# Kernel optimization log

Hardware: AMD Instinct MI355X
Metric: run time of the kernel (lower is better)

Reference implementation:

```python
import jax, jax.numpy as jnp
import numpy as np

N = 20000      # nodes
E = 320000     # directed edges (avg degree 16)
H = 4          # GAT attention heads
IN, HID, OUT = 5, 64, 32
DIMS = [(HID, HID), (HID, HID), (HID, OUT)]  # per-layer (in, out_per_head)


def setup_inputs() -> dict:
    keys = iter(jax.random.split(jax.random.key(0), 64))

    def rn(shape, s=0.1):
        return jax.random.normal(next(keys), shape, jnp.float32) * s

    inp = {
        "x": jax.random.normal(next(keys), (N, IN), jnp.float32),
        "edge_index": jax.random.randint(next(keys), (2, E), 0, N, dtype=jnp.int32),
        "enc_W": rn((IN, HID)), "enc_b": rn((HID,)),
    }
    for l, (din, dout) in enumerate(DIMS):
        inp["W%d" % l] = rn((din, H * dout))
        inp["as%d" % l] = rn((H, dout))
        inp["ad%d" % l] = rn((H, dout))
        inp["b%d" % l] = rn((dout,))
        inp["g%d" % l] = 1.0 + rn((dout,))
        inp["be%d" % l] = rn((dout,))
        inp["m%d" % l] = rn((dout,))
        inp["v%d" % l] = 1.0 + 0.1 * jax.random.uniform(next(keys), (dout,), jnp.float32)
    for h in ("eth", "man"):
        inp[h + "_W1"] = rn((OUT, OUT // 2)); inp[h + "_b1"] = rn((OUT // 2,))
        inp[h + "_W2"] = rn((OUT // 2, 1)); inp[h + "_b2"] = rn((1,))
    return inp


def _gat(x, src, dst, W, a_s, a_d, bias, n):
    # PyG GATConv: heads=H, concat=False (head mean), leaky_relu slope 0.2
    xp = (x @ W).reshape(n, H, -1)                        # [N,H,C]
    al_s = (xp * a_s).sum(-1)                             # [N,H]
    al_d = (xp * a_d).sum(-1)                             # [N,H]
    e = jax.nn.leaky_relu(al_s[src] + al_d[dst], 0.2)     # [E',H]
    emax = jax.ops.segment_max(e, dst, num_segments=n)    # stable softmax over in-edges
    ee = jnp.exp(e - emax[dst])
    den = jax.ops.segment_sum(ee, dst, num_segments=n)
    alpha = ee / (den[dst] + 1e-16)                       # [E',H]
    out = jax.ops.segment_sum(alpha[:, :, None] * xp[src], dst, num_segments=n)
    return out.mean(axis=1) + bias                        # [N,C]


def _bn(x, g, b, m, v):
    # BatchNorm1d, eval mode with running stats
    return (x - m) / jnp.sqrt(v + 1e-5) * g + b


def _head(z, W1, b1, W2, b2):
    # Linear -> ReLU -> (dropout off) -> Linear -> Sigmoid
    return jax.nn.sigmoid(jax.nn.relu(z @ W1 + b1) @ W2 + b2)


def _forward(x, src, dst, enc_W, enc_b, Ws, ASs, ADs, Bs, Gs, BEs, Ms, Vs, eth, man):
    n = x.shape[0]
    h = x @ enc_W + enc_b
    for l in range(3):
        h = _gat(h, src, dst, Ws[l], ASs[l], ADs[l], Bs[l], n)
        h = _bn(h, Gs[l], BEs[l], Ms[l], Vs[l])
        if l < 2:
            h = jax.nn.relu(h)
    graph_emb = h.mean(axis=0, keepdims=True)             # no `batch` attr branch
    ethics = _head(graph_emb, *eth)
    manip = _head(graph_emb, *man)
    return h, graph_emb, ethics, manip


def reference(x, edge_index, enc_W, enc_b,
              W0, as0, ad0, b0, g0, be0, m0, v0,
              W1, as1, ad1, b1, g1, be1, m1, v1,
              W2, as2, ad2, b2, g2, be2, m2, v2,
              eth_W1, eth_b1, eth_W2, eth_b2,
              man_W1, man_b1, man_W2, man_b2):
    n = x.shape[0]
    loops = jnp.arange(n, dtype=edge_index.dtype)
    src = jnp.concatenate([edge_index[0], loops])         # GATConv adds self-loops
    dst = jnp.concatenate([edge_index[1], loops])
    return _forward(x, src, dst, enc_W, enc_b,
                    [W0, W1, W2], [as0, as1, as2], [ad0, ad1, ad2], [b0, b1, b2],
                    [g0, g1, g2], [be0, be1, be2], [m0, m1, m2], [v0, v1, v2],
                    (eth_W1, eth_b1, eth_W2, eth_b2),
                    (man_W1, man_b1, man_W2, man_b2))
```

## Files before the change

### kernel.cpp

```cpp
#include <hip/hip_runtime.h>
#include <math.h>


#define H4 4

static __device__ __forceinline__ unsigned short f2bf(float f) {
  unsigned u = __float_as_uint(f);
  u += 0x7fffu + ((u >> 16) & 1u);
  return (unsigned short)(u >> 16);
}

static __device__ __forceinline__ float bfh(unsigned u) {
  return __uint_as_float(u << 16);
}
static __device__ __forceinline__ float bfl(unsigned u) {
  return __uint_as_float(u & 0xffff0000u);
}

__global__ void k_count(const int* __restrict__ dst, int* __restrict__ deg, int E) {
  int gid = blockIdx.x * blockDim.x + threadIdx.x;
  if (gid < E) atomicAdd(&deg[dst[gid]], 1);
}

__global__ void k_alloc(int* __restrict__ cursor, int* __restrict__ rbeg,
                        int* __restrict__ rend, int* __restrict__ col,
                        int* __restrict__ counter, float* __restrict__ gacc, int N) {
  int gid = blockIdx.x * blockDim.x + threadIdx.x;
  int lane = threadIdx.x & 63;
  if (gid < 32) gacc[gid] = 0.f;
  int size = (gid < N) ? (cursor[gid] + 1) : 0;
  int v = size;
#pragma unroll
  for (int off = 1; off < 64; off <<= 1) {
    int t = __shfl_up(v, off, 64);
    if (lane >= off) v += t;
  }
  int tot = __shfl(v, 63, 64);
  int base = 0;
  if (lane == 63) base = atomicAdd(counter, tot);
  base = __shfl(base, 63, 64);
  if (gid < N) {
    int p = base + v - size;
    rbeg[gid] = p;
    rend[gid] = p + size;
    col[p] = gid;
    cursor[gid] = p + 1;
  }
}

__global__ void k_scatter(const int* __restrict__ src, const int* __restrict__ dst,
                          int* __restrict__ cursor, int* __restrict__ col, int E) {
  int gid = blockIdx.x * blockDim.x + threadIdx.x;
  if (gid < E) {
    int p = atomicAdd(&cursor[dst[gid]], 1);
    col[p] = src[gid];
  }
}

template <int HC, bool ENC>
__global__ void k_gemm_al(const float* __restrict__ hin,
                          const float* __restrict__ encW, const float* __restrict__ encb,
                          const float* __restrict__ W,
                          const float* __restrict__ a_s, const float* __restrict__ a_d,
                          unsigned short* __restrict__ xpb,
                          float* __restrict__ als, float* __restrict__ ald, int N) {
  constexpr int K = 64, NB = 16, C = HC / H4;
  __shared__ float hs[NB * K];
  int n0 = blockIdx.x * NB;
  int tid = threadIdx.x;
  if (ENC) {
    for (int idx = tid; idx < NB * K; idx += HC) {
      int i = idx >> 6, j = idx & 63;
      int n = n0 + i;
      float a = 0.f;
      if (n < N) {
        a = encb[j];
#pragma unroll
        for (int k = 0; k < 5; ++k) a += hin[n * 5 + k] * encW[k * 64 + j];
      }
      hs[idx] = a;
    }
  } else {
    for (int idx = tid; idx < NB * K; idx += HC) {
      int n = n0 + (idx >> 6);
      hs[idx] = (n < N) ? hin[(size_t)n0 * K + idx] : 0.f;
    }
  }
  __syncthreads();
  float acc[NB];
#pragma unroll
  for (int i = 0; i < NB; ++i) acc[i] = 0.f;
  for (int k = 0; k < K; k += 4) {
    float w0 = W[(k + 0) * HC + tid];
    float w1 = W[(k + 1) * HC + tid];
    float w2 = W[(k + 2) * HC + tid];
    float w3 = W[(k + 3) * HC + tid];
#pragma unroll
    for (int i = 0; i < NB; ++i) {
      float4 hv = *(const float4*)&hs[i * K + k];
      acc[i] += hv.x * w0 + hv.y * w1 + hv.z * w2 + hv.w * w3;
    }
  }
#pragma unroll
  for (int i = 0; i < NB; ++i) {
    int n = n0 + i;
    if (n < N) xpb[(size_t)n * HC + tid] = f2bf(acc[i]);
  }
  float as_w = a_s[tid], ad_w = a_d[tid];
  int c = tid & (C - 1);
  int h = tid / C;
#pragma unroll
  for (int i = 0; i < NB; ++i) {
    float vs = acc[i] * as_w, vd = acc[i] * ad_w;
#pragma unroll
    for (int off = C >> 1; off; off >>= 1) {
      vs += __shfl_xor(vs, off, 64);
      vd += __shfl_xor(vd, off, 64);
    }
    int n = n0 + i;
    if (c == 0 && n < N) {
      als[n * H4 + h] = vs;
      ald[n * H4 + h] = vd;
    }
  }
}

template <int C, bool RELU>
__global__ void k_gather(const unsigned short* __restrict__ xpb,
                         const float* __restrict__ als, const float* __restrict__ ald,
                         const int* __restrict__ rbeg, const int* __restrict__ rend,
                         const int* __restrict__ col,
                         const float* __restrict__ bias, const float* __restrict__ g,
                         const float* __restrict__ be, const float* __restrict__ m,
                         const float* __restrict__ v, float* __restrict__ hout, int N) {
  constexpr int HC = H4 * C;
  constexpr int VPL = HC / 64;
  int wave = threadIdx.x >> 6;
  int lane = threadIdx.x & 63;
  int n = blockIdx.x * 2 + wave;
  if (n >= N) return;
  int h = lane >> 4;
  float aldn = ald[n * H4 + h];
  int beg = rbeg[n], end = rend[n];

  float s = 0.f;
  float acc[VPL];
#pragma unroll
  for (int i = 0; i < VPL; ++i) acc[i] = 0.f;

  int j = beg;
  for (; j + 3 < end; j += 4) {
    int s0 = col[j], s1 = col[j + 1], s2 = col[j + 2], s3 = col[j + 3];
    float a0 = als[s0 * H4 + h], a1 = als[s1 * H4 + h];
    float a2 = als[s2 * H4 + h], a3 = als[s3 * H4 + h];
    float e0 = a0 + aldn; e0 = (e0 > 0.f) ? e0 : 0.2f * e0; e0 = __expf(e0);
    float e1 = a1 + aldn; e1 = (e1 > 0.f) ? e1 : 0.2f * e1; e1 = __expf(e1);
    float e2 = a2 + aldn; e2 = (e2 > 0.f) ? e2 : 0.2f * e2; e2 = __expf(e2);
    float e3 = a3 + aldn; e3 = (e3 > 0.f) ? e3 : 0.2f * e3; e3 = __expf(e3);
    s += (e0 + e1) + (e2 + e3);
    if constexpr (VPL == 4) {
      uint2 u0 = *(const uint2*)(xpb + (size_t)s0 * HC + lane * 4);
      uint2 u1 = *(const uint2*)(xpb + (size_t)s1 * HC + lane * 4);
      uint2 u2 = *(const uint2*)(xpb + (size_t)s2 * HC + lane * 4);
      uint2 u3 = *(const uint2*)(xpb + (size_t)s3 * HC + lane * 4);
      acc[0] += e0 * bfh(u0.x) + e1 * bfh(u1.x) + e2 * bfh(u2.x) + e3 * bfh(u3.x);
      acc[1] += e0 * bfl(u0.x) + e1 * bfl(u1.x) + e2 * bfl(u2.x) + e3 * bfl(u3.x);
      acc[2] += e0 * bfh(u0.y) + e1 * bfh(u1.y) + e2 * bfh(u2.y) + e3 * bfh(u3.y);
      acc[3] += e0 * bfl(u0.y) + e1 * bfl(u1.y) + e2 * bfl(u2.y) + e3 * bfl(u3.y);
    } else {
      unsigned u0 = *(const unsigned*)(xpb + (size_t)s0 * HC + lane * 2);
      unsigned u1 = *(const unsigned*)(xpb + (size_t)s1 * HC + lane * 2);
      unsigned u2 = *(const unsigned*)(xpb + (size_t)s2 * HC + lane * 2);
      unsigned u3 = *(const unsigned*)(xpb + (size_t)s3 * HC + lane * 2);
      acc[0] += e0 * bfh(u0) + e1 * bfh(u1) + e2 * bfh(u2) + e3 * bfh(u3);
      acc[1] += e0 * bfl(u0) + e1 * bfl(u1) + e2 * bfl(u2) + e3 * bfl(u3);
    }
  }
  for (; j < end; ++j) {
    int s0 = col[j];
    float a0 = als[s0 * H4 + h];
    float e0 = a0 + aldn; e0 = (e0 > 0.f) ? e0 : 0.2f * e0; e0 = __expf(e0);
    s += e0;
    if constexpr (VPL == 4) {
      uint2 u0 = *(const uint2*)(xpb + (size_t)s0 * HC + lane * 4);
      acc[0] += e0 * bfh(u0.x);
      acc[1] += e0 * bfl(u0.x);
      acc[2] += e0 * bfh(u0.y);
      acc[3] += e0 * bfl(u0.y);
    } else {
      unsigned u0 = *(const unsigned*)(xpb + (size_t)s0 * HC + lane * 2);
      acc[0] += e0 * bfh(u0);
      acc[1] += e0 * bfl(u0);
    }
  }

  float inv = 1.f / (s + 1e-16f);
#pragma unroll
  for (int i = 0; i < VPL; ++i) {
    acc[i] *= inv;
    acc[i] += __shfl_xor(acc[i], 16, 64);
    acc[i] += __shfl_xor(acc[i], 32, 64);
  }

  if (lane < 16) {
    int c0 = lane * VPL;
    float o[VPL];
#pragma unroll
    for (int i = 0; i < VPL; ++i) {
      int cc = c0 + i;
      float t = acc[i] * (1.f / H4) + bias[cc];
      t = (t - m[cc]) * rsqrtf(v[cc] + 1e-5f) * g[cc] + be[cc];
      if (RELU) t = fmaxf(t, 0.f);
      o[i] = t;
    }
    if constexpr (VPL == 4)
      *(float4*)&hout[(size_t)n * C + c0] = make_float4(o[0], o[1], o[2], o[3]);
    else
      *(float2*)&hout[(size_t)n * C + c0] = make_float2(o[0], o[1]);
  }
}

__global__ void k_reduce_heads(const float* __restrict__ hfin, float* __restrict__ gacc,
                               int* __restrict__ ticket,
                               const float* __restrict__ eW1, const float* __restrict__ eb1,
                               const float* __restrict__ eW2, const float* __restrict__ eb2,
                               const float* __restrict__ mW1, const float* __restrict__ mb1,
                               const float* __restrict__ mW2, const float* __restrict__ mb2,
                               float* __restrict__ out, int N) {
  __shared__ float lds[256];
  __shared__ bool last;
  int tid = threadIdx.x;
  int c = tid & 31;
  int rowStart = blockIdx.x * (blockDim.x / 32) + (tid >> 5);
  int rowStride = gridDim.x * (blockDim.x / 32);
  float acc = 0.f;
  for (int n = rowStart; n < N; n += rowStride) acc += hfin[(size_t)n * 32 + c];
  lds[tid] = acc;
  __syncthreads();
  if (tid < 32) {
    float s = 0.f;
#pragma unroll
    for (int i = 0; i < 8; ++i) s += lds[i * 32 + tid];
    atomicAdd(&gacc[tid], s);
  }
  __threadfence();
  __syncthreads();
  if (tid == 0) last = (atomicAdd(ticket, 1) == (int)gridDim.x - 1);
  __syncthreads();
  if (!last) return;

  __shared__ float z[32];
  __shared__ float hid[32];
  size_t base = (size_t)N * 32;
  if (tid < 32) {
    float zv = atomicAdd(&gacc[tid], 0.f) / (float)N;
    z[tid] = zv;
    out[base + tid] = zv;
  }
  __syncthreads();
  if (tid < 16) {
    float a = eb1[tid], b = mb1[tid];
    for (int k = 0; k < 32; ++k) {
      a += z[k] * eW1[k * 16 + tid];
      b += z[k] * mW1[k * 16 + tid];
    }
    hid[tid] = fmaxf(a, 0.f);
    hid[16 + tid] = fmaxf(b, 0.f);
  }
  __syncthreads();
  if (tid == 0) {
    float a = eb2[0];
    for (int k = 0; k < 16; ++k) a += hid[k] * eW2[k];
    out[base + 32] = 1.f / (1.f + __expf(-a));
  } else if (tid == 1) {
    float a = mb2[0];
    for (int k = 0; k < 16; ++k) a += hid[16 + k] * mW2[k];
    out[base + 33] = 1.f / (1.f + __expf(-a));
  }
}

extern "C" void kernel_launch(void* const* d_in, const int* in_sizes, int n_in,
                              void* d_out, int out_size, void* d_ws, size_t ws_size,
                              hipStream_t stream) {
  const int N = in_sizes[0] / 5;
  const int E = in_sizes[1] / 2;
  const int M = E + N;

  const float* x = (const float*)d_in[0];
  const int* ei = (const int*)d_in[1];
  const int* e_src = ei;
  const int* e_dst = ei + E;
  const float* encW = (const float*)d_in[2];
  const float* encb = (const float*)d_in[3];
  const float* Wl[3]; const float* asl[3]; const float* adl[3]; const float* bl[3];
  const float* gl[3]; const float* bel[3]; const float* ml[3]; const float* vl[3];
  for (int l = 0; l < 3; ++l) {
    const int o = 4 + 8 * l;
    Wl[l]  = (const float*)d_in[o + 0];
    asl[l] = (const float*)d_in[o + 1];
    adl[l] = (const float*)d_in[o + 2];
    bl[l]  = (const float*)d_in[o + 3];
    gl[l]  = (const float*)d_in[o + 4];
    bel[l] = (const float*)d_in[o + 5];
    ml[l]  = (const float*)d_in[o + 6];
    vl[l]  = (const float*)d_in[o + 7];
  }
  const float* eW1 = (const float*)d_in[28];
  const float* eb1 = (const float*)d_in[29];
  const float* eW2 = (const float*)d_in[30];
  const float* eb2 = (const float*)d_in[31];
  const float* mW1 = (const float*)d_in[32];
  const float* mb1 = (const float*)d_in[33];
  const float* mW2 = (const float*)d_in[34];
  const float* mb2 = (const float*)d_in[35];

  float* out = (float*)d_out;

  float* wf = (float*)d_ws;
  size_t off = 0;
  float* hA   = wf + off; off += (size_t)N * 64;
  float* hB   = wf + off; off += (size_t)N * 64;
  unsigned short* xpb = (unsigned short*)(wf + off); off += (size_t)N * 128;
  float* als  = wf + off; off += (size_t)N * 4;
  float* ald  = wf + off; off += (size_t)N * 4;
  float* gacc = wf + off; off += 32;
  int* wi = (int*)(wf + off);
  int* col     = wi;
  int* rbeg    = col + M;
  int* rend    = rbeg + N;
  int* cursor  = rend + N;
  int* counter = cursor + N;
  int* ticket  = counter + 1;

  const int T = 256;
  const int gE  = (E + T - 1) / T;
  const int gN  = (N + T - 1) / T;
  const int gGE = (N + 15) / 16;
  const int gGA = (N + 1) / 2;

  hipMemsetAsync(cursor, 0, (size_t)(N + 2) * sizeof(int), stream);
  k_count<<<gE, T, 0, stream>>>(e_dst, cursor, E);
  k_alloc<<<gN, T, 0, stream>>>(cursor, rbeg, rend, col, counter, gacc, N);
  k_scatter<<<gE, T, 0, stream>>>(e_src, e_dst, cursor, col, E);

  k_gemm_al<256, true><<<gGE, 256, 0, stream>>>(x, encW, encb, Wl[0], asl[0], adl[0],
                                                xpb, als, ald, N);
  k_gather<64, true><<<gGA, 128, 0, stream>>>(xpb, als, ald, rbeg, rend, col,
                                              bl[0], gl[0], bel[0], ml[0], vl[0], hB, N);

  k_gemm_al<256, false><<<gGE, 256, 0, stream>>>(hB, encW, encb, Wl[1], asl[1], adl[1],
                                                 xpb, als, ald, N);
  k_gather<64, true><<<gGA, 128, 0, stream>>>(xpb, als, ald, rbeg, rend, col,
                                              bl[1], gl[1], bel[1], ml[1], vl[1], hA, N);

  k_gemm_al<128, false><<<gGE, 128, 0, stream>>>(hA, encW, encb, Wl[2], asl[2], adl[2],
                                                 xpb, als, ald, N);
  k_gather<32, false><<<gGA, 128, 0, stream>>>(xpb, als, ald, rbeg, rend, col,
                                               bl[2], gl[2], bel[2], ml[2], vl[2], out, N);

  k_reduce_heads<<<80, 256, 0, stream>>>(out, gacc, ticket,
                                         eW1, eb1, eW2, eb2, mW1, mb1, mW2, mb2, out, N);
}
```

Baseline: 343.5 us.

## Split node gather across two waves, precompose attention vectors, fuse pooling into gather

Each gather block now handles one node with two waves that each take half of the in-edge list, then combine partial sums through shared memory. The goal is to shorten per-node latency and balance work across waves. Attention logits are now computed as h·(W·a) with the folded vectors built once in k_alloc, replacing the per-column shuffle reductions. Graph mean pooling is folded into the last gather via atomics into 256 partial buckets, removing a separate pass over the output. In exchange, block count doubles with a __syncthreads per node, and per-element atomics add contention.

Measured after the change: 332.9 us. -3.1%, faster.

```diff
diff --git a/kernel.cpp b/kernel.cpp
--- a/kernel.cpp
+++ b/kernel.cpp
@@ -24,10 +24,13 @@
 
 __global__ void k_alloc(int* __restrict__ cursor, int* __restrict__ rbeg,
                         int* __restrict__ rend, int* __restrict__ col,
-                        int* __restrict__ counter, float* __restrict__ gacc, int N) {
+                        int* __restrict__ counter, int N,
+                        const float* __restrict__ W0, const float* __restrict__ as0, const float* __restrict__ ad0,
+                        const float* __restrict__ W1, const float* __restrict__ as1, const float* __restrict__ ad1,
+                        const float* __restrict__ W2, const float* __restrict__ as2, const float* __restrict__ ad2,
+                        float* __restrict__ pas, float* __restrict__ pad) {
   int gid = blockIdx.x * blockDim.x + threadIdx.x;
   int lane = threadIdx.x & 63;
-  if (gid < 32) gacc[gid] = 0.f;
   int size = (gid < N) ? (cursor[gid] + 1) : 0;
   int v = size;
 #pragma unroll
@@ -46,6 +49,24 @@
     col[p] = gid;
     cursor[gid] = p + 1;
   }
+  if (blockIdx.x < 3) {
+    int l = blockIdx.x;
+    const float* W  = (l == 0) ? W0 : (l == 1) ? W1 : W2;
+    const float* ap = (l == 0) ? as0 : (l == 1) ? as1 : as2;
+    const float* dp = (l == 0) ? ad0 : (l == 1) ? ad1 : ad2;
+    int HC = (l == 2) ? 128 : 256;
+    int C  = HC / H4;
+    int tid = threadIdx.x;
+    int k = tid >> 2, h = tid & 3;
+    float vs = 0.f, vd = 0.f;
+    for (int c = 0; c < C; ++c) {
+      float w = W[k * HC + h * C + c];
+      vs += w * ap[h * C + c];
+      vd += w * dp[h * C + c];
+    }
+    pas[l * 256 + tid] = vs;
+    pad[l * 256 + tid] = vd;
+  }
 }
 
 __global__ void k_scatter(const int* __restrict__ src, const int* __restrict__ dst,
@@ -61,10 +82,10 @@
 __global__ void k_gemm_al(const float* __restrict__ hin,
                           const float* __restrict__ encW, const float* __restrict__ encb,
                           const float* __restrict__ W,
-                          const float* __restrict__ a_s, const float* __restrict__ a_d,
+                          const float* __restrict__ was, const float* __restrict__ wad,
                           unsigned short* __restrict__ xpb,
                           float* __restrict__ als, float* __restrict__ ald, int N) {
-  constexpr int K = 64, NB = 16, C = HC / H4;
+  constexpr int K = 64, NB = 16;
   __shared__ float hs[NB * K];
   int n0 = blockIdx.x * NB;
   int tid = threadIdx.x;
@@ -106,50 +127,55 @@
     int n = n0 + i;
     if (n < N) xpb[(size_t)n * HC + tid] = f2bf(acc[i]);
   }
-  float as_w = a_s[tid], ad_w = a_d[tid];
-  int c = tid & (C - 1);
-  int h = tid / C;
-#pragma unroll
-  for (int i = 0; i < NB; ++i) {
-    float vs = acc[i] * as_w, vd = acc[i] * ad_w;
-#pragma unroll
-    for (int off = C >> 1; off; off >>= 1) {
-      vs += __shfl_xor(vs, off, 64);
-      vd += __shfl_xor(vd, off, 64);
-    }
+  if (tid < NB * H4) {
+    int i = tid >> 2, h = tid & 3;
     int n = n0 + i;
-    if (c == 0 && n < N) {
+    float vs = 0.f, vd = 0.f;
+#pragma unroll 8
+    for (int k = 0; k < K; ++k) {
+      float hv = hs[i * K + k];
+      vs += hv * was[k * 4 + h];
+      vd += hv * wad[k * 4 + h];
+    }
+    if (n < N) {
       als[n * H4 + h] = vs;
       ald[n * H4 + h] = vd;
     }
   }
 }
 
-template <int C, bool RELU>
-__global__ void k_gather(const unsigned short* __restrict__ xpb,
-                         const float* __restrict__ als, const float* __restrict__ ald,
-                         const int* __restrict__ rbeg, const int* __restrict__ rend,
-                         const int* __restrict__ col,
-                         const float* __restrict__ bias, const float* __restrict__ g,
-                         const float* __restrict__ be, const float* __restrict__ m,
-                         const float* __restrict__ v, float* __restrict__ hout, int N) {
+template <int C, bool RELU, bool POOL>
+__global__ __launch_bounds__(128) void k_gather(
+    const unsigned short* __restrict__ xpb,
+    const float* __restrict__ als, const float* __restrict__ ald,
+    const int* __restrict__ rbeg, const int* __restrict__ rend,
+    const int* __restrict__ col,
+    const float* __restrict__ bias, const float* __restrict__ g,
+    const float* __restrict__ be, const float* __restrict__ m,
+    const float* __restrict__ v, float* __restrict__ hout,
+    float* __restrict__ gpart, int N) {
   constexpr int HC = H4 * C;
   constexpr int VPL = HC / 64;
-  int wave = threadIdx.x >> 6;
+  __shared__ float accbuf[HC];
+  __shared__ float sbuf[H4];
+  int sub = threadIdx.x >> 6;
   int lane = threadIdx.x & 63;
-  int n = blockIdx.x * 2 + wave;
-  if (n >= N) return;
+  int n = blockIdx.x;
   int h = lane >> 4;
   float aldn = ald[n * H4 + h];
   int beg = rbeg[n], end = rend[n];
+  int len = end - beg;
+  int lenA = (len + 1) >> 1;
+  int jb = sub ? (beg + lenA) : beg;
+  int je = sub ? end : (beg + lenA);
 
   float s = 0.f;
   float acc[VPL];
 #pragma unroll
   for (int i = 0; i < VPL; ++i) acc[i] = 0.f;
 
-  int j = beg;
-  for (; j + 3 < end; j += 4) {
+  int j = jb;
+  for (; j + 3 < je; j += 4) {
     int s0 = col[j], s1 = col[j + 1], s2 = col[j + 2], s3 = col[j + 3];
     float a0 = als[s0 * H4 + h], a1 = als[s1 * H4 + h];
     float a2 = als[s2 * H4 + h], a3 = als[s3 * H4 + h];
@@ -176,7 +202,7 @@
       acc[1] += e0 * bfl(u0) + e1 * bfl(u1) + e2 * bfl(u2) + e3 * bfl(u3);
     }
   }
-  for (; j < end; ++j) {
+  for (; j < je; ++j) {
     int s0 = col[j];
     float a0 = als[s0 * H4 + h];
     float e0 = a0 + aldn; e0 = (e0 > 0.f) ? e0 : 0.2f * e0; e0 = __expf(e0);
@@ -194,6 +220,17 @@
     }
   }
 
+  if (sub) {
+    if ((lane & 15) == 0) sbuf[h] = s;
+#pragma unroll
+    for (int i = 0; i < VPL; ++i) accbuf[lane * VPL + i] = acc[i];
+  }
+  __syncthreads();
+  if (sub) return;
+  s += sbuf[h];
+#pragma unroll
+  for (int i = 0; i < VPL; ++i) acc[i] += accbuf[lane * VPL + i];
+
   float inv = 1.f / (s + 1e-16f);
 #pragma unroll
   for (int i = 0; i < VPL; ++i) {
@@ -212,6 +249,7 @@
       t = (t - m[cc]) * rsqrtf(v[cc] + 1e-5f) * g[cc] + be[cc];
       if (RELU) t = fmaxf(t, 0.f);
       o[i] = t;
+      if (POOL) atomicAdd(&gpart[(blockIdx.x & 255) * 32 + cc], t);
     }
     if constexpr (VPL == 4)
       *(float4*)&hout[(size_t)n * C + c0] = make_float4(o[0], o[1], o[2], o[3]);
@@ -220,42 +258,29 @@
   }
 }
 
-__global__ void k_reduce_heads(const float* __restrict__ hfin, float* __restrict__ gacc,
-                               int* __restrict__ ticket,
-                               const float* __restrict__ eW1, const float* __restrict__ eb1,
-                               const float* __restrict__ eW2, const float* __restrict__ eb2,
-                               const float* __restrict__ mW1, const float* __restrict__ mb1,
-                               const float* __restrict__ mW2, const float* __restrict__ mb2,
-                               float* __restrict__ out, int N) {
-  __shared__ float lds[256];
-  __shared__ bool last;
+__global__ void k_heads2(const float* __restrict__ gpart,
+                         const float* __restrict__ eW1, const float* __restrict__ eb1,
+                         const float* __restrict__ eW2, const float* __restrict__ eb2,
+                         const float* __restrict__ mW1, const float* __restrict__ mb1,
+                         const float* __restrict__ mW2, const float* __restrict__ mb2,
+                         float* __restrict__ out, int N) {
+  __shared__ float red[256];
+  __shared__ float z[32];
+  __shared__ float hid[32];
   int tid = threadIdx.x;
   int c = tid & 31;
-  int rowStart = blockIdx.x * (blockDim.x / 32) + (tid >> 5);
-  int rowStride = gridDim.x * (blockDim.x / 32);
-  float acc = 0.f;
-  for (int n = rowStart; n < N; n += rowStride) acc += hfin[(size_t)n * 32 + c];
-  lds[tid] = acc;
-  __syncthreads();
-  if (tid < 32) {
-    float s = 0.f;
-#pragma unroll
-    for (int i = 0; i < 8; ++i) s += lds[i * 32 + tid];
-    atomicAdd(&gacc[tid], s);
-  }
-  __threadfence();
-  __syncthreads();
-  if (tid == 0) last = (atomicAdd(ticket, 1) == (int)gridDim.x - 1);
-  __syncthreads();
-  if (!last) return;
-
-  __shared__ float z[32];
-  __shared__ float hid[32];
+  float s = 0.f;
+  for (int b = tid >> 5; b < 256; b += 8) s += gpart[b * 32 + c];
+  red[tid] = s;
+  __syncthreads();
   size_t base = (size_t)N * 32;
   if (tid < 32) {
-    float zv = atomicAdd(&gacc[tid], 0.f) / (float)N;
-    z[tid] = zv;
-    out[base + tid] = zv;
+    float t = 0.f;
+#pragma unroll
+    for (int i = 0; i < 8; ++i) t += red[i * 32 + tid];
+    t /= (float)N;
+    z[tid] = t;
+    out[base + tid] = t;
   }
   __syncthreads();
   if (tid < 16) {
@@ -323,41 +348,45 @@
   unsigned short* xpb = (unsigned short*)(wf + off); off += (size_t)N * 128;
   float* als  = wf + off; off += (size_t)N * 4;
   float* ald  = wf + off; off += (size_t)N * 4;
-  float* gacc = wf + off; off += 32;
+  float* pas  = wf + off; off += 3 * 256;
+  float* pad  = wf + off; off += 3 * 256;
   int* wi = (int*)(wf + off);
   int* col     = wi;
   int* rbeg    = col + M;
   int* rend    = rbeg + N;
   int* cursor  = rend + N;
   int* counter = cursor + N;
-  int* ticket  = counter + 1;
+  float* gpart = (float*)(counter + 1);
 
   const int T = 256;
   const int gE  = (E + T - 1) / T;
   const int gN  = (N + T - 1) / T;
   const int gGE = (N + 15) / 16;
-  const int gGA = (N + 1) / 2;
-
-  hipMemsetAsync(cursor, 0, (size_t)(N + 2) * sizeof(int), stream);
+
+  hipMemsetAsync(cursor, 0, (size_t)(N + 1) * sizeof(int) + 256 * 32 * sizeof(float), stream);
   k_count<<<gE, T, 0, stream>>>(e_dst, cursor, E);
-  k_alloc<<<gN, T, 0, stream>>>(cursor, rbeg, rend, col, counter, gacc, N);
+  k_alloc<<<gN, T, 0, stream>>>(cursor, rbeg, rend, col, counter, N,
+                                Wl[0], asl[0], adl[0], Wl[1], asl[1], adl[1],
+                                Wl[2], asl[2], adl[2], pas, pad);
   k_scatter<<<gE, T, 0, stream>>>(e_src, e_dst, cursor, col, E);
 
-  k_gemm_al<256, true><<<gGE, 256, 0, stream>>>(x, encW, encb, Wl[0], asl[0], adl[0],
+  k_gemm_al<256, true><<<gGE, 256, 0, stream>>>(x, encW, encb, Wl[0], pas, pad,
                                                 xpb, als, ald, N);
-  k_gather<64, true><<<gGA, 128, 0, stream>>>(xpb, als, ald, rbeg, rend, col,
-                                              bl[0], gl[0], bel[0], ml[0], vl[0], hB, N);
-
-  k_gemm_al<256, false><<<gGE, 256, 0, stream>>>(hB, encW, encb, Wl[1], asl[1], adl[1],
+  k_gather<64, true, false><<<N, 128, 0, stream>>>(xpb, als, ald, rbeg, rend, col,
+                                                   bl[0], gl[0], bel[0], ml[0], vl[0],
+                                                   hB, gpart, N);
+
+  k_gemm_al<256, false><<<gGE, 256, 0, stream>>>(hB, encW, encb, Wl[1], pas + 256, pad + 256,
                                                  xpb, als, ald, N);
-  k_gather<64, true><<<gGA, 128, 0, stream>>>(xpb, als, ald, rbeg, rend, col,
-                                              bl[1], gl[1], bel[1], ml[1], vl[1], hA, N);
-
-  k_gemm_al<128, false><<<gGE, 128, 0, stream>>>(hA, encW, encb, Wl[2], asl[2], adl[2],
+  k_gather<64, true, false><<<N, 128, 0, stream>>>(xpb, als, ald, rbeg, rend, col,
+                                                   bl[1], gl[1], bel[1], ml[1], vl[1],
+                                                   hA, gpart, N);
+
+  k_gemm_al<128, false><<<gGE, 128, 0, stream>>>(hA, encW, encb, Wl[2], pas + 512, pad + 512,
                                                  xpb, als, ald, N);
-  k_gather<32, false><<<gGA, 128, 0, stream>>>(xpb, als, ald, rbeg, rend, col,
-                                               bl[2], gl[2], bel[2], ml[2], vl[2], out, N);
-
-  k_reduce_heads<<<80, 256, 0, stream>>>(out, gacc, ticket,
-                                         eW1, eb1, eW2, eb2, mW1, mb1, mW2, mb2, out, N);
-}
+  k_gather<32, false, true><<<N, 128, 0, stream>>>(xpb, als, ald, rbeg, rend, col,
+                                                   bl[2], gl[2], bel[2], ml[2], vl[2],
+                                                   out, gpart, N);
+
+  k_heads2<<<1, 256, 0, stream>>>(gpart, eW1, eb1, eW2, eb2, mW1, mb1, mW2, mb2, out, N);
+}
```
